# Performance work log

Measured on AMD Instinct MI355X. Metric: run time of the kernel, lower is better.

The kernel has to match this reference:

```python
import jax, jax.numpy as jnp
import numpy as np
from jax import lax

ITERATIONS = 10
B, I, D, J, E = 512, 7, 512, 64, 128


def setup_inputs() -> dict:
    key = jax.random.key(0)
    k1, k2, k3 = jax.random.split(key, 3)
    f_bid = jax.random.normal(k1, (B, I, D), dtype=jnp.float32)
    p_bi = jax.random.uniform(k2, (B, I), dtype=jnp.float32)
    weights = jax.random.normal(k3, (I, D, J, E), dtype=jnp.float32)
    return {"f_bid": f_bid, "p_bi": p_bi, "weights": weights}


def reference(f_bid, p_bi, weights):
    # Precompute the per-capsule vote tensor once: [B, I, J, E]
    f_W_bije = jnp.einsum('bid,idje->bije', f_bid, weights)
    b = f_bid.shape[0]
    j, e = weights.shape[2], weights.shape[3]
    c0 = jnp.ones((b, j, e), dtype=f_bid.dtype)

    def body(c_bj, _):
        # routing logits over output capsules j, softmax over j (dim=-1 of 'bij')
        r_bij = jax.nn.softmax(jnp.einsum('bije,bje->bij', f_W_bije, c_bj), axis=-1)
        c_next = jnp.einsum('bi,bij,bije->bje', p_bi, r_bij, f_W_bije)
        return c_next, r_bij

    c_bj, r_stack = lax.scan(body, c0, None, length=ITERATIONS)
    return c_bj, r_stack[-1]
```

## Files before the change

### kernel.cpp

```cpp
#include <hip/hip_runtime.h>
#include <hip/hip_bf16.h>

#define B_SZ 512
#define I_SZ 7
#define D_SZ 512
#define J_SZ 64
#define E_SZ 128
#define N_SZ 8192
#define ITERS 10

typedef __attribute__((ext_vector_type(8))) short bf16x8;
typedef __attribute__((ext_vector_type(4))) float f32x4;

#define AST 40
#define BST 40

__device__ inline void split_bf16(float x, short& h, short& l) {
    union { float f; unsigned u; } v; v.f = x;
    unsigned r = v.u + 0x7FFF + ((v.u >> 16) & 1);
    unsigned short hu = (unsigned short)(r >> 16);
    h = (short)hu;
    union { unsigned u; float f; } hb; hb.u = ((unsigned)hu) << 16;
    float res = x - hb.f;
    v.f = res;
    r = v.u + 0x7FFF + ((v.u >> 16) & 1);
    l = (short)(r >> 16);
}

__global__ __launch_bounds__(256) void vote_gemm_mfma(
    const float* __restrict__ f,
    const float* __restrict__ W,
    float* __restrict__ fW)
{
    const int i  = blockIdx.z;
    const int m0 = blockIdx.y * 128;
    const int n0 = blockIdx.x * 128;
    const int th = threadIdx.x;

    __shared__ short As_hi[128 * AST], As_lo[128 * AST];
    __shared__ short Bs_hi[128 * BST], Bs_lo[128 * BST];

    const int am  = th >> 1;
    const int akg = th & 1;
    const int bn  = th & 127;
    const int bkh = th >> 7;

    const float* fA = f + (size_t)(m0 + am) * (I_SZ * D_SZ) + (size_t)i * D_SZ + akg * 16;
    const float* WB = W + (size_t)i * D_SZ * N_SZ + n0 + bn;

    const int wave = th >> 6, lane = th & 63;
    const int wr = wave >> 1, wc = wave & 1;
    const int lm = lane & 15, quad = lane >> 4;

    f32x4 acc[4][4];
#pragma unroll
    for (int a = 0; a < 4; ++a)
#pragma unroll
        for (int c = 0; c < 4; ++c)
            acc[a][c] = (f32x4){0.f, 0.f, 0.f, 0.f};

    for (int k0 = 0; k0 < D_SZ; k0 += 32) {
        float av[16];
        {
            const float* pa = fA + k0;
            float4 t0 = *(const float4*)(pa);
            float4 t1 = *(const float4*)(pa + 4);
            float4 t2 = *(const float4*)(pa + 8);
            float4 t3 = *(const float4*)(pa + 12);
            av[0]=t0.x; av[1]=t0.y; av[2]=t0.z; av[3]=t0.w;
            av[4]=t1.x; av[5]=t1.y; av[6]=t1.z; av[7]=t1.w;
            av[8]=t2.x; av[9]=t2.y; av[10]=t2.z; av[11]=t2.w;
            av[12]=t3.x; av[13]=t3.y; av[14]=t3.z; av[15]=t3.w;
        }
        float bv[16];
        {
            const float* pb = WB + (size_t)(k0 + bkh * 16) * N_SZ;
#pragma unroll
            for (int r = 0; r < 16; ++r) bv[r] = pb[(size_t)r * N_SZ];
        }

        bf16x8 ah0, ah1, al0, al1, bh0, bh1, bl0, bl1;
#pragma unroll
        for (int u = 0; u < 8; ++u) {
            short h, l;
            split_bf16(av[u], h, l);      ah0[u] = h; al0[u] = l;
            split_bf16(av[u + 8], h, l);  ah1[u] = h; al1[u] = l;
            split_bf16(bv[u], h, l);      bh0[u] = h; bl0[u] = l;
            split_bf16(bv[u + 8], h, l);  bh1[u] = h; bl1[u] = l;
        }

        __syncthreads();
        *(bf16x8*)&As_hi[am * AST + akg * 16]     = ah0;
        *(bf16x8*)&As_hi[am * AST + akg * 16 + 8] = ah1;
        *(bf16x8*)&As_lo[am * AST + akg * 16]     = al0;
        *(bf16x8*)&As_lo[am * AST + akg * 16 + 8] = al1;
        *(bf16x8*)&Bs_hi[bn * BST + bkh * 16]     = bh0;
        *(bf16x8*)&Bs_hi[bn * BST + bkh * 16 + 8] = bh1;
        *(bf16x8*)&Bs_lo[bn * BST + bkh * 16]     = bl0;
        *(bf16x8*)&Bs_lo[bn * BST + bkh * 16 + 8] = bl1;
        __syncthreads();

        bf16x8 Ah[4], Al[4], Bh[4], Bl[4];
#pragma unroll
        for (int t = 0; t < 4; ++t) {
            const int ar = (wr * 64 + t * 16 + lm) * AST + quad * 8;
            Ah[t] = *(const bf16x8*)&As_hi[ar];
            Al[t] = *(const bf16x8*)&As_lo[ar];
            const int br = (wc * 64 + t * 16 + lm) * BST + quad * 8;
            Bh[t] = *(const bf16x8*)&Bs_hi[br];
            Bl[t] = *(const bf16x8*)&Bs_lo[br];
        }
#pragma unroll
        for (int tm = 0; tm < 4; ++tm)
#pragma unroll
            for (int tn = 0; tn < 4; ++tn) {
                acc[tm][tn] = __builtin_amdgcn_mfma_f32_16x16x32_bf16(Ah[tm], Bh[tn], acc[tm][tn], 0, 0, 0);
                acc[tm][tn] = __builtin_amdgcn_mfma_f32_16x16x32_bf16(Ah[tm], Bl[tn], acc[tm][tn], 0, 0, 0);
                acc[tm][tn] = __builtin_amdgcn_mfma_f32_16x16x32_bf16(Al[tm], Bh[tn], acc[tm][tn], 0, 0, 0);
            }
    }

#pragma unroll
    for (int tm = 0; tm < 4; ++tm) {
        const int rowb = m0 + wr * 64 + tm * 16 + quad * 4;
#pragma unroll
        for (int tn = 0; tn < 4; ++tn) {
            const int col = n0 + wc * 64 + tn * 16 + lm;
#pragma unroll
            for (int r = 0; r < 4; ++r)
                fW[((size_t)(rowb + r) * I_SZ + i) * N_SZ + col] = acc[tm][tn][r];
        }
    }
}

__global__ __launch_bounds__(1024) void routing_kernel(
    const float* __restrict__ fW,
    const float* __restrict__ p,
    float* __restrict__ c_out,
    float* __restrict__ r_out)
{
    const int b   = blockIdx.x;
    const int tid = threadIdx.x;
    const int j   = tid >> 4;
    const int sub = tid & 15;

    __shared__ float G_sh[64][49];
    __shared__ float s_sh[64][9];
    __shared__ float w_sh[2][64][9];
    __shared__ float p_sh[8];

    if (tid < I_SZ) p_sh[tid] = p[(size_t)b * I_SZ + tid];

    float4 fw[I_SZ][2];
    const float* base = fW + (size_t)b * I_SZ * N_SZ + j * E_SZ + sub * 8;
#pragma unroll
    for (int i = 0; i < I_SZ; ++i) {
        fw[i][0] = *(const float4*)(base + (size_t)i * N_SZ);
        fw[i][1] = *(const float4*)(base + (size_t)i * N_SZ + 4);
    }

#pragma unroll
    for (int i = 0; i < I_SZ; ++i) {
        float s = fw[i][0].x + fw[i][0].y + fw[i][0].z + fw[i][0].w
                + fw[i][1].x + fw[i][1].y + fw[i][1].z + fw[i][1].w;
        s += __shfl_xor(s, 1); s += __shfl_xor(s, 2);
        s += __shfl_xor(s, 4); s += __shfl_xor(s, 8);
        if (sub == 0) s_sh[j][i] = s;
#pragma unroll
        for (int i2 = i; i2 < I_SZ; ++i2) {
            float g = fw[i][0].x * fw[i2][0].x + fw[i][0].y * fw[i2][0].y
                    + fw[i][0].z * fw[i2][0].z + fw[i][0].w * fw[i2][0].w
                    + fw[i][1].x * fw[i2][1].x + fw[i][1].y * fw[i2][1].y
                    + fw[i][1].z * fw[i2][1].z + fw[i][1].w * fw[i2][1].w;
            g += __shfl_xor(g, 1); g += __shfl_xor(g, 2);
            g += __shfl_xor(g, 4); g += __shfl_xor(g, 8);
            if (sub == 0) { G_sh[j][i * 7 + i2] = g; G_sh[j][i2 * 7 + i] = g; }
        }
    }
    __syncthreads();

    for (int t = 0; t < ITERS; ++t) {
        if (tid < I_SZ * 64) {
            const int ii = tid >> 6;
            const int jj = tid & 63;
            float l;
            if (t == 0) {
                l = s_sh[jj][ii];
            } else {
                const int rb = t & 1;
                l = 0.f;
#pragma unroll
                for (int i2 = 0; i2 < I_SZ; ++i2)
                    l = fmaf(w_sh[rb][jj][i2], G_sh[jj][ii * 7 + i2], l);
            }
            float mx = l;
#pragma unroll
            for (int off = 32; off > 0; off >>= 1)
                mx = fmaxf(mx, __shfl_xor(mx, off));
            float ex = __expf(l - mx);
            float sm = ex;
#pragma unroll
            for (int off = 32; off > 0; off >>= 1)
                sm += __shfl_xor(sm, off);
            float r = ex / sm;
            if (t == ITERS - 1)
                r_out[(size_t)b * (I_SZ * J_SZ) + ii * 64 + jj] = r;
            w_sh[(t + 1) & 1][jj][ii] = p_sh[ii] * r;
        }
        __syncthreads();
    }

    float4 a0 = make_float4(0.f, 0.f, 0.f, 0.f);
    float4 a1 = make_float4(0.f, 0.f, 0.f, 0.f);
#pragma unroll
    for (int i = 0; i < I_SZ; ++i) {
        float wv = w_sh[ITERS & 1][j][i];
        a0.x = fmaf(wv, fw[i][0].x, a0.x); a0.y = fmaf(wv, fw[i][0].y, a0.y);
        a0.z = fmaf(wv, fw[i][0].z, a0.z); a0.w = fmaf(wv, fw[i][0].w, a0.w);
        a1.x = fmaf(wv, fw[i][1].x, a1.x); a1.y = fmaf(wv, fw[i][1].y, a1.y);
        a1.z = fmaf(wv, fw[i][1].z, a1.z); a1.w = fmaf(wv, fw[i][1].w, a1.w);
    }
    float* dst = c_out + (size_t)b * N_SZ + j * E_SZ + sub * 8;
    *(float4*)(dst)     = a0;
    *(float4*)(dst + 4) = a1;
}

extern "C" void kernel_launch(void* const* d_in, const int* in_sizes, int n_in,
                              void* d_out, int out_size, void* d_ws, size_t ws_size,
                              hipStream_t stream) {
    const float* f = (const float*)d_in[0];
    const float* p = (const float*)d_in[1];
    const float* W = (const float*)d_in[2];
    float* out = (float*)d_out;
    float* fW  = (float*)d_ws;

    vote_gemm_mfma<<<dim3(N_SZ / 128, B_SZ / 128, I_SZ), 256, 0, stream>>>(f, W, fW);
    routing_kernel<<<B_SZ, 1024, 0, stream>>>(fW, p, out, out + (size_t)B_SZ * N_SZ);
}
```

Measured before the change: 348.5 us.

## Prefetch next K-tile into registers and use packed bf16 split conversion

The GEMM main loop now loads the next K-slice of f and W into registers right after the shared-memory store barrier, so global-load latency overlaps the MFMA work on the current tile. The fp32-to-bf16 hi/lo split is rewritten to process pairs, using the hardware packed bf16 conversion builtin when the compiler provides it and a perm-based packing fallback otherwise. The aim is to hide memory latency and cut ALU instructions in the conversion, at the cost of higher register pressure from holding the prefetched values across the MFMA block.

```diff
diff --git a/kernel.cpp b/kernel.cpp
--- a/kernel.cpp
+++ b/kernel.cpp
@@ -15,16 +15,36 @@
 #define AST 40
 #define BST 40
 
-__device__ inline void split_bf16(float x, short& h, short& l) {
-    union { float f; unsigned u; } v; v.f = x;
-    unsigned r = v.u + 0x7FFF + ((v.u >> 16) & 1);
-    unsigned short hu = (unsigned short)(r >> 16);
-    h = (short)hu;
-    union { unsigned u; float f; } hb; hb.u = ((unsigned)hu) << 16;
-    float res = x - hb.f;
-    v.f = res;
-    r = v.u + 0x7FFF + ((v.u >> 16) & 1);
-    l = (short)(r >> 16);
+#if defined(__has_builtin)
+#if __has_builtin(__builtin_amdgcn_cvt_pk_bf16_f32)
+#define HAVE_CVT_PK_BF16 1
+#endif
+#endif
+
+__device__ inline void split2(float x0, float x1, unsigned& hp, unsigned& lp) {
+#ifdef HAVE_CVT_PK_BF16
+    auto h = __builtin_amdgcn_cvt_pk_bf16_f32(x0, x1);
+    hp = __builtin_bit_cast(unsigned, h);
+    union { unsigned u; float f; } b0, b1;
+    b0.u = hp << 16;
+    b1.u = hp & 0xFFFF0000u;
+    auto l = __builtin_amdgcn_cvt_pk_bf16_f32(x0 - b0.f, x1 - b1.f);
+    lp = __builtin_bit_cast(unsigned, l);
+#else
+    union { float f; unsigned u; } u0, u1;
+    u0.f = x0; u1.f = x1;
+    unsigned r0 = u0.u + 0x7FFF + ((u0.u >> 16) & 1);
+    unsigned r1 = u1.u + 0x7FFF + ((u1.u >> 16) & 1);
+    hp = __builtin_amdgcn_perm(r1, r0, 0x07060302);
+    union { unsigned u; float f; } h0, h1;
+    h0.u = r0 & 0xFFFF0000u;
+    h1.u = r1 & 0xFFFF0000u;
+    union { float f; unsigned u; } s0, s1;
+    s0.f = x0 - h0.f; s1.f = x1 - h1.f;
+    unsigned q0 = s0.u + 0x7FFF + ((s0.u >> 16) & 1);
+    unsigned q1 = s1.u + 0x7FFF + ((s1.u >> 16) & 1);
+    lp = __builtin_amdgcn_perm(q1, q0, 0x07060302);
+#endif
 }
 
 __global__ __launch_bounds__(256) void vote_gemm_mfma(
@@ -59,10 +79,53 @@
         for (int c = 0; c < 4; ++c)
             acc[a][c] = (f32x4){0.f, 0.f, 0.f, 0.f};
 
+    float av[16], bv[16];
+    {
+        float4 t0 = *(const float4*)(fA);
+        float4 t1 = *(const float4*)(fA + 4);
+        float4 t2 = *(const float4*)(fA + 8);
+        float4 t3 = *(const float4*)(fA + 12);
+        av[0]=t0.x; av[1]=t0.y; av[2]=t0.z; av[3]=t0.w;
+        av[4]=t1.x; av[5]=t1.y; av[6]=t1.z; av[7]=t1.w;
+        av[8]=t2.x; av[9]=t2.y; av[10]=t2.z; av[11]=t2.w;
+        av[12]=t3.x; av[13]=t3.y; av[14]=t3.z; av[15]=t3.w;
+        const float* pb = WB + (size_t)(bkh * 16) * N_SZ;
+#pragma unroll
+        for (int r = 0; r < 16; ++r) bv[r] = pb[(size_t)r * N_SZ];
+    }
+
     for (int k0 = 0; k0 < D_SZ; k0 += 32) {
-        float av[16];
-        {
-            const float* pa = fA + k0;
+        uint4 ah0, al0, ah1, al1, bh0, bl0, bh1, bl1;
+        split2(av[0],  av[1],  ah0.x, al0.x);
+        split2(av[2],  av[3],  ah0.y, al0.y);
+        split2(av[4],  av[5],  ah0.z, al0.z);
+        split2(av[6],  av[7],  ah0.w, al0.w);
+        split2(av[8],  av[9],  ah1.x, al1.x);
+        split2(av[10], av[11], ah1.y, al1.y);
+        split2(av[12], av[13], ah1.z, al1.z);
+        split2(av[14], av[15], ah1.w, al1.w);
+        split2(bv[0],  bv[1],  bh0.x, bl0.x);
+        split2(bv[2],  bv[3],  bh0.y, bl0.y);
+        split2(bv[4],  bv[5],  bh0.z, bl0.z);
+        split2(bv[6],  bv[7],  bh0.w, bl0.w);
+        split2(bv[8],  bv[9],  bh1.x, bl1.x);
+        split2(bv[10], bv[11], bh1.y, bl1.y);
+        split2(bv[12], bv[13], bh1.z, bl1.z);
+        split2(bv[14], bv[15], bh1.w, bl1.w);
+
+        __syncthreads();
+        *(uint4*)&As_hi[am * AST + akg * 16]     = ah0;
+        *(uint4*)&As_hi[am * AST + akg * 16 + 8] = ah1;
+        *(uint4*)&As_lo[am * AST + akg * 16]     = al0;
+        *(uint4*)&As_lo[am * AST + akg * 16 + 8] = al1;
+        *(uint4*)&Bs_hi[bn * BST + bkh * 16]     = bh0;
+        *(uint4*)&Bs_hi[bn * BST + bkh * 16 + 8] = bh1;
+        *(uint4*)&Bs_lo[bn * BST + bkh * 16]     = bl0;
+        *(uint4*)&Bs_lo[bn * BST + bkh * 16 + 8] = bl1;
+        __syncthreads();
+
+        if (k0 + 32 < D_SZ) {
+            const float* pa = fA + k0 + 32;
             float4 t0 = *(const float4*)(pa);
             float4 t1 = *(const float4*)(pa + 4);
             float4 t2 = *(const float4*)(pa + 8);
@@ -71,34 +134,10 @@
             av[4]=t1.x; av[5]=t1.y; av[6]=t1.z; av[7]=t1.w;
             av[8]=t2.x; av[9]=t2.y; av[10]=t2.z; av[11]=t2.w;
             av[12]=t3.x; av[13]=t3.y; av[14]=t3.z; av[15]=t3.w;
-        }
-        float bv[16];
-        {
-            const float* pb = WB + (size_t)(k0 + bkh * 16) * N_SZ;
+            const float* pb = WB + (size_t)(k0 + 32 + bkh * 16) * N_SZ;
 #pragma unroll
             for (int r = 0; r < 16; ++r) bv[r] = pb[(size_t)r * N_SZ];
         }
-
-        bf16x8 ah0, ah1, al0, al1, bh0, bh1, bl0, bl1;
-#pragma unroll
-        for (int u = 0; u < 8; ++u) {
-            short h, l;
-            split_bf16(av[u], h, l);      ah0[u] = h; al0[u] = l;
-            split_bf16(av[u + 8], h, l);  ah1[u] = h; al1[u] = l;
-            split_bf16(bv[u], h, l);      bh0[u] = h; bl0[u] = l;
-            split_bf16(bv[u + 8], h, l);  bh1[u] = h; bl1[u] = l;
-        }
-
-        __syncthreads();
-        *(bf16x8*)&As_hi[am * AST + akg * 16]     = ah0;
-        *(bf16x8*)&As_hi[am * AST + akg * 16 + 8] = ah1;
-        *(bf16x8*)&As_lo[am * AST + akg * 16]     = al0;
-        *(bf16x8*)&As_lo[am * AST + akg * 16 + 8] = al1;
-        *(bf16x8*)&Bs_hi[bn * BST + bkh * 16]     = bh0;
-        *(bf16x8*)&Bs_hi[bn * BST + bkh * 16 + 8] = bh1;
-        *(bf16x8*)&Bs_lo[bn * BST + bkh * 16]     = bl0;
-        *(bf16x8*)&Bs_lo[bn * BST + bkh * 16 + 8] = bl1;
-        __syncthreads();
 
         bf16x8 Ah[4], Al[4], Bh[4], Bl[4];
 #pragma unroll
```

Measured after the change: 288.5 us. 1.21x faster.
